# Kernel optimization log

Hardware: AMD Instinct MI355X
Metric: run time of the kernel (lower is better)

## Reference

```python
import jax, jax.numpy as jnp
import numpy as np


def setup_inputs() -> dict:
    key = jax.random.key(0)
    kx, kw = jax.random.split(key)
    B, IN, OUT = 8192, 4096, 4096
    x = jax.random.normal(kx, (B, IN), dtype=jnp.float32)
    # matches torch init: (rand*2-1)*0.001 -> uniform in [-0.001, 0.001]
    weight = jax.random.uniform(kw, (OUT, IN), dtype=jnp.float32, minval=-1.0, maxval=1.0) * 0.001
    return {"x": x, "weight": weight}


def reference(x, weight):
    # scaling factor = mean(|W|), detached
    scale = jax.lax.stop_gradient(jnp.mean(jnp.abs(weight)))
    binary_no_grad = scale * jnp.sign(weight)
    clipped = jnp.clip(weight, -1.0, 1.0)
    # straight-through estimator: fwd value = scale*sign(W), bwd grad = d(clip)/dW
    binary_weights = jax.lax.stop_gradient(binary_no_grad - clipped) + clipped
    # F.linear: y = x @ W^T  -> [B, OUT]
    return jnp.einsum('bi,oi->bo', x, binary_weights)
```

## Files before the change

### kernel.cpp

```cpp
#include <hip/hip_runtime.h>
#include <hip/hip_bf16.h>
#include <stdint.h>

typedef __attribute__((ext_vector_type(4))) int i32x4;
typedef __attribute__((ext_vector_type(4))) float f32x4;

#define GLOAD(g, l) __builtin_amdgcn_global_load_lds(                      \
    (const __attribute__((address_space(1))) void*)(g),                    \
    (__attribute__((address_space(3))) void*)(l), 16, 0, 0)

#define MFMAI8 __builtin_amdgcn_mfma_i32_16x16x64_i8
#define BARRIER __builtin_amdgcn_s_barrier

__global__ __launch_bounds__(512, 2) void gemm_i8_kernel(
    const char* __restrict__ A,
    const char* __restrict__ B,
    const float* __restrict__ partials, const float* __restrict__ qrow,
    float* __restrict__ C) {
  constexpr int M = 8192, N = 4096, K = 4096;
  constexpr int NT = K / 128;
  constexpr int NI = NT / 2;
  __shared__ __align__(16) char lds[131072];

  const int tid = threadIdx.x;
  const int wid = tid >> 6;
  const int lane = tid & 63;
  const int wr = wid >> 2;
  const int wc = wid & 3;
  const int bh = wc >> 1;
  const int bsub = (wc & 1) * 8192;
  const int fr = lane & 15;
  const int fq = lane >> 4;
  const int sk0 = ((fq) ^ (fr & 7)) * 16;
  const int sk1 = ((4 + fq) ^ (fr & 7)) * 16;

  const int bid = blockIdx.x;
  const int xcd = bid & 7;
  const int local = bid >> 3;
  const int tm = (xcd >> 1) * 8 + (local >> 3);
  const int tn = (xcd & 1) * 8 + (local & 7);

  const int srow = tid >> 3;
  const int sg = (tid & 7) ^ (srow & 7);
  const char* aSrc0 = A + (size_t)(tm * 256 + srow) * K + sg * 16;
  const char* aSrc1 = aSrc0 + (size_t)128 * K;
  const char* bSrc0 = B + (size_t)(tn * 256 + srow) * K + sg * 16;
  const char* bSrc1 = bSrc0 + (size_t)128 * K;

#define STAGE(srcBase, slotIdx, koff)                              \
  do {                                                             \
    const char* _s = (srcBase) + (koff);                           \
    char* _d = lds + (slotIdx) * 16384 + wid * 1024;               \
    GLOAD(_s, _d);                                                 \
    GLOAD(_s + (size_t)64 * K, _d + 8192);                         \
  } while (0)

  const char* aSp0 = lds + (0 + wr) * 16384 + fr * 128;
  const char* aSp1 = lds + (2 + wr) * 16384 + fr * 128;
  const char* bSp0 = lds + (4 + bh) * 16384 + bsub + fr * 128;
  const char* bSp1 = lds + (6 + bh) * 16384 + bsub + fr * 128;

  i32x4 acc[8][4];
#pragma unroll
  for (int m = 0; m < 8; ++m)
#pragma unroll
    for (int n = 0; n < 4; ++n) acc[m][n] = (i32x4){0, 0, 0, 0};

#define RD_B(bS)                                                       \
  _Pragma("unroll") for (int n = 0; n < 4; ++n) {                      \
    bq[n][0] = *(const i32x4*)((bS) + n * 2048 + sk0);                 \
    bq[n][1] = *(const i32x4*)((bS) + n * 2048 + sk1);                 \
  }
#define RD_A(dst, aS, q)                                               \
  _Pragma("unroll") for (int m2 = 0; m2 < 2; ++m2) {                   \
    dst[m2][0] = *(const i32x4*)((aS) + (2 * (q) + m2) * 2048 + sk0);  \
    dst[m2][1] = *(const i32x4*)((aS) + (2 * (q) + m2) * 2048 + sk1);  \
  }
#define QMFMA(av, q)                                                   \
  do {                                                                 \
    __builtin_amdgcn_s_setprio(1);                                     \
    _Pragma("unroll") for (int m2 = 0; m2 < 2; ++m2)                   \
        _Pragma("unroll") for (int n = 0; n < 4; ++n) {                \
      acc[2 * (q) + m2][n] =                                           \
          MFMAI8(av[m2][0], bq[n][0], acc[2 * (q) + m2][n], 0, 0, 0);  \
      acc[2 * (q) + m2][n] =                                           \
          MFMAI8(av[m2][1], bq[n][1], acc[2 * (q) + m2][n], 0, 0, 0);  \
    }                                                                  \
    __builtin_amdgcn_s_setprio(0);                                     \
  } while (0)

  STAGE(bSrc0, 4, 0);
  STAGE(bSrc1, 5, 0);
  STAGE(aSrc0, 0, 0);
  STAGE(aSrc1, 1, 0);
  STAGE(bSrc0, 6, 128);
  asm volatile("s_waitcnt vmcnt(2)" ::: "memory");
  BARRIER();

  i32x4 bq[4][2], av0[2][2], av1[2][2];
  RD_B(bSp0);
  RD_A(av0, aSp0, 0);

  for (int i = 0; i < NI; ++i) {
    const int t0 = 2 * i;
    const int k1 = (t0 + 1) * 128, k2 = (t0 + 2) * 128, k3 = (t0 + 3) * 128;

    RD_A(av1, aSp0, 1);
    STAGE(bSrc1, 7, k1);
    BARRIER();
    QMFMA(av0, 0);

    RD_A(av0, aSp0, 2);
    STAGE(aSrc0, 2, k1);
    BARRIER();
    QMFMA(av1, 1);

    RD_A(av1, aSp0, 3);
    STAGE(aSrc1, 3, k1);
    BARRIER();
    QMFMA(av0, 2);

    if (t0 + 2 < NT) {
      STAGE(bSrc0, 4, k2);
      asm volatile("s_waitcnt vmcnt(2)" ::: "memory");
    } else {
      asm volatile("s_waitcnt vmcnt(0)" ::: "memory");
    }
    BARRIER();
    QMFMA(av1, 3);
    RD_B(bSp1);
    RD_A(av0, aSp1, 0);

    RD_A(av1, aSp1, 1);
    if (t0 + 2 < NT) STAGE(bSrc1, 5, k2);
    BARRIER();
    QMFMA(av0, 0);

    RD_A(av0, aSp1, 2);
    if (t0 + 2 < NT) STAGE(aSrc0, 0, k2);
    BARRIER();
    QMFMA(av1, 1);

    RD_A(av1, aSp1, 3);
    if (t0 + 2 < NT) STAGE(aSrc1, 1, k2);
    BARRIER();
    QMFMA(av0, 2);

    if (t0 + 2 < NT) {
      STAGE(bSrc0, 6, k3);
      asm volatile("s_waitcnt vmcnt(2)" ::: "memory");
    }
    BARRIER();
    QMFMA(av1, 3);
    if (t0 + 2 < NT) {
      RD_B(bSp0);
      RD_A(av0, aSp0, 0);
    }
  }

  BARRIER();
  float s = 0.f;
  for (int i = tid; i < 4096; i += 512) s += partials[i];
#pragma unroll
  for (int off = 32; off > 0; off >>= 1) s += __shfl_down(s, off, 64);
  float* smf = reinterpret_cast<float*>(lds);
  if (lane == 0) smf[wid] = s;
  BARRIER();
  float tot = 0.f;
#pragma unroll
  for (int j = 0; j < 8; ++j) tot += smf[j];
  const float sc = tot * (1.0f / 16777216.0f);

  const int crow0 = tm * 256 + wr * 128 + fq * 4;
  const int ccol0 = tn * 256 + wc * 64 + fr;
#pragma unroll
  for (int m = 0; m < 8; ++m) {
    const int row = crow0 + m * 16;
    float q[4];
#pragma unroll
    for (int j = 0; j < 4; ++j) q[j] = sc * qrow[row + j];
#pragma unroll
    for (int n = 0; n < 4; ++n) {
      i32x4 v = acc[m][n];
      float* cp = C + (size_t)row * N + ccol0 + n * 16;
#pragma unroll
      for (int j = 0; j < 4; ++j) cp[(size_t)j * N] = (float)v[j] * q[j];
    }
  }
#undef STAGE
#undef RD_A
#undef RD_B
#undef QMFMA
}

__global__ __launch_bounds__(256) void prep_kernel(
    const float* __restrict__ X, const float* __restrict__ W,
    char* __restrict__ XQ, char* __restrict__ SQ,
    float* __restrict__ qrow, float* __restrict__ partials) {
  const int b = blockIdx.x;
  const int tid = threadIdx.x;
  if (b < 8192) {
    const int row = b;
    const f32x4* xr =
        reinterpret_cast<const f32x4*>(X + (size_t)row * 4096);
    int* xo = reinterpret_cast<int*>(XQ + (size_t)row * 4096);
    f32x4 v[4];
    float am = 0.f;
#pragma unroll
    for (int i = 0; i < 4; ++i) {
      v[i] = __builtin_nontemporal_load(xr + tid + 256 * i);
      am = fmaxf(am, fmaxf(fmaxf(fabsf(v[i][0]), fabsf(v[i][1])),
                           fmaxf(fabsf(v[i][2]), fabsf(v[i][3]))));
    }
#pragma unroll
    for (int off = 1; off < 64; off <<= 1)
      am = fmaxf(am, __shfl_xor(am, off, 64));
    __shared__ float wm[4];
    if ((tid & 63) == 0) wm[tid >> 6] = am;
    __syncthreads();
    float amax = fmaxf(fmaxf(wm[0], wm[1]), fmaxf(wm[2], wm[3]));
    amax = fmaxf(amax, 1e-20f);
    const float rq = 127.f / amax;
#pragma unroll
    for (int i = 0; i < 4; ++i) {
      int b0 = __float2int_rn(v[i][0] * rq);
      int b1 = __float2int_rn(v[i][1] * rq);
      int b2 = __float2int_rn(v[i][2] * rq);
      int b3 = __float2int_rn(v[i][3] * rq);
      xo[tid + 256 * i] = (b0 & 255) | ((b1 & 255) << 8) |
                          ((b2 & 255) << 16) | ((b3 & 255) << 24);
    }
    if (tid == 0) qrow[row] = amax * (1.f / 127.f);
  } else {
    const int base = (b - 8192) * 1024;
    const f32x4* wp = reinterpret_cast<const f32x4*>(W);
    int* sp = reinterpret_cast<int*>(SQ);
    float s = 0.f;
#pragma unroll
    for (int i = 0; i < 4; ++i) {
      const int idx = base + tid + 256 * i;
      f32x4 w = __builtin_nontemporal_load(wp + idx);
      int b0 = (w[0] > 0.f) - (w[0] < 0.f);
      int b1 = (w[1] > 0.f) - (w[1] < 0.f);
      int b2 = (w[2] > 0.f) - (w[2] < 0.f);
      int b3 = (w[3] > 0.f) - (w[3] < 0.f);
      sp[idx] = (b0 & 255) | ((b1 & 255) << 8) | ((b2 & 255) << 16) |
                ((b3 & 255) << 24);
      s += fabsf(w[0]) + fabsf(w[1]) + fabsf(w[2]) + fabsf(w[3]);
    }
#pragma unroll
    for (int off = 32; off > 0; off >>= 1) s += __shfl_down(s, off, 64);
    __shared__ float sm[4];
    if ((tid & 63) == 0) sm[tid >> 6] = s;
    __syncthreads();
    if (tid == 0) partials[b - 8192] = sm[0] + sm[1] + sm[2] + sm[3];
  }
}

extern "C" void kernel_launch(void* const* d_in, const int* in_sizes, int n_in,
                              void* d_out, int out_size, void* d_ws,
                              size_t ws_size, hipStream_t stream) {
  const float* x = (const float*)d_in[0];
  const float* w = (const float*)d_in[1];
  float* out = (float*)d_out;

  char* ws = (char*)d_ws;
  char* xq = ws;
  char* sq = ws + 33554432;
  float* qrow = (float*)(ws + 50331648);
  float* partials = (float*)(ws + 50331648 + 32768);

  prep_kernel<<<12288, 256, 0, stream>>>(x, w, xq, sq, qrow, partials);
  gemm_i8_kernel<<<512, 512, 0, stream>>>(xq, sq, partials, qrow, out);
}
```

Baseline: 161.5 us.

## Load A operand directly from global into registers, stage only B in LDS

The A tile is no longer staged through LDS. Each wave now reads its A fragments straight from global memory into registers. Only B is double-buffered in LDS, which halves the shared-memory footprint and reduces barriers to roughly two per k-step. The aim is to cut LDS traffic and synchronisation. The cost is that the four waves sharing an A row block each fetch it separately, and the per-lane 16-byte strided global reads are less coalesced, which raises L2/global load pressure and exposes more latency to the MFMA chain.

```diff
diff --git a/kernel.cpp b/kernel.cpp
--- a/kernel.cpp
+++ b/kernel.cpp
@@ -19,8 +19,7 @@
     float* __restrict__ C) {
   constexpr int M = 8192, N = 4096, K = 4096;
   constexpr int NT = K / 128;
-  constexpr int NI = NT / 2;
-  __shared__ __align__(16) char lds[131072];
+  __shared__ __align__(16) char lds[65536];
 
   const int tid = threadIdx.x;
   const int wid = tid >> 6;
@@ -42,8 +41,6 @@
 
   const int srow = tid >> 3;
   const int sg = (tid & 7) ^ (srow & 7);
-  const char* aSrc0 = A + (size_t)(tm * 256 + srow) * K + sg * 16;
-  const char* aSrc1 = aSrc0 + (size_t)128 * K;
   const char* bSrc0 = B + (size_t)(tn * 256 + srow) * K + sg * 16;
   const char* bSrc1 = bSrc0 + (size_t)128 * K;
 
@@ -55,10 +52,15 @@
     GLOAD(_s + (size_t)64 * K, _d + 8192);                         \
   } while (0)
 
-  const char* aSp0 = lds + (0 + wr) * 16384 + fr * 128;
-  const char* aSp1 = lds + (2 + wr) * 16384 + fr * 128;
-  const char* bSp0 = lds + (4 + bh) * 16384 + bsub + fr * 128;
-  const char* bSp1 = lds + (6 + bh) * 16384 + bsub + fr * 128;
+  const char* bSp0 = lds + bh * 16384 + bsub + fr * 128;
+
+  const char* aRow = A + (size_t)(tm * 256 + wr * 128 + fr) * K + fq * 16;
+
+#define LD_A(dst, q, koff)                                              \
+  _Pragma("unroll") for (int m2 = 0; m2 < 2; ++m2)                      \
+      _Pragma("unroll") for (int kk = 0; kk < 2; ++kk)                  \
+          dst[m2][kk] = *(const i32x4*)(aRow +                          \
+              (size_t)(2 * (q) + m2) * 16 * K + (koff) + kk * 64);
 
   i32x4 acc[8][4];
 #pragma unroll
@@ -70,11 +72,6 @@
   _Pragma("unroll") for (int n = 0; n < 4; ++n) {                      \
     bq[n][0] = *(const i32x4*)((bS) + n * 2048 + sk0);                 \
     bq[n][1] = *(const i32x4*)((bS) + n * 2048 + sk1);                 \
-  }
-#define RD_A(dst, aS, q)                                               \
-  _Pragma("unroll") for (int m2 = 0; m2 < 2; ++m2) {                   \
-    dst[m2][0] = *(const i32x4*)((aS) + (2 * (q) + m2) * 2048 + sk0);  \
-    dst[m2][1] = *(const i32x4*)((aS) + (2 * (q) + m2) * 2048 + sk1);  \
   }
 #define QMFMA(av, q)                                                   \
   do {                                                                 \
@@ -89,75 +86,47 @@
     __builtin_amdgcn_s_setprio(0);                                     \
   } while (0)
 
-  STAGE(bSrc0, 4, 0);
-  STAGE(bSrc1, 5, 0);
-  STAGE(aSrc0, 0, 0);
-  STAGE(aSrc1, 1, 0);
-  STAGE(bSrc0, 6, 128);
-  asm volatile("s_waitcnt vmcnt(2)" ::: "memory");
+  i32x4 bq[4][2], av0[2][2], av1[2][2];
+
+  STAGE(bSrc0, 0, 0);
+  STAGE(bSrc1, 1, 0);
+  STAGE(bSrc0, 2, 128);
+  STAGE(bSrc1, 3, 128);
+  LD_A(av0, 0, 0);
+  asm volatile("s_waitcnt vmcnt(8)" ::: "memory");
   BARRIER();
 
-  i32x4 bq[4][2], av0[2][2], av1[2][2];
-  RD_B(bSp0);
-  RD_A(av0, aSp0, 0);
-
-  for (int i = 0; i < NI; ++i) {
-    const int t0 = 2 * i;
-    const int k1 = (t0 + 1) * 128, k2 = (t0 + 2) * 128, k3 = (t0 + 3) * 128;
-
-    RD_A(av1, aSp0, 1);
-    STAGE(bSrc1, 7, k1);
+  for (int t = 0; t < NT; ++t) {
+    const int par = t & 1;
+    const char* bS = bSp0 + par * 32768;
+    const int koff = t * 128;
+
+    RD_B(bS);
+    LD_A(av1, 1, koff);
+    QMFMA(av0, 0);
+
+    LD_A(av0, 2, koff);
+    QMFMA(av1, 1);
+
     BARRIER();
-    QMFMA(av0, 0);
-
-    RD_A(av0, aSp0, 2);
-    STAGE(aSrc0, 2, k1);
-    BARRIER();
-    QMFMA(av1, 1);
-
-    RD_A(av1, aSp0, 3);
-    STAGE(aSrc1, 3, k1);
-    BARRIER();
+
+    LD_A(av1, 3, koff);
+    if (t + 2 < NT) {
+      STAGE(bSrc0, par * 2, (t + 2) * 128);
+      STAGE(bSrc1, par * 2 + 1, (t + 2) * 128);
+    }
     QMFMA(av0, 2);
 
-    if (t0 + 2 < NT) {
-      STAGE(bSrc0, 4, k2);
-      asm volatile("s_waitcnt vmcnt(2)" ::: "memory");
-    } else {
-      asm volatile("s_waitcnt vmcnt(0)" ::: "memory");
-    }
-    BARRIER();
+    if (t + 1 < NT) LD_A(av0, 0, (t + 1) * 128);
     QMFMA(av1, 3);
-    RD_B(bSp1);
-    RD_A(av0, aSp1, 0);
-
-    RD_A(av1, aSp1, 1);
-    if (t0 + 2 < NT) STAGE(bSrc1, 5, k2);
-    BARRIER();
-    QMFMA(av0, 0);
-
-    RD_A(av0, aSp1, 2);
-    if (t0 + 2 < NT) STAGE(aSrc0, 0, k2);
-    BARRIER();
-    QMFMA(av1, 1);
-
-    RD_A(av1, aSp1, 3);
-    if (t0 + 2 < NT) STAGE(aSrc1, 1, k2);
-    BARRIER();
-    QMFMA(av0, 2);
-
-    if (t0 + 2 < NT) {
-      STAGE(bSrc0, 6, k3);
-      asm volatile("s_waitcnt vmcnt(2)" ::: "memory");
-    }
-    BARRIER();
-    QMFMA(av1, 3);
-    if (t0 + 2 < NT) {
-      RD_B(bSp0);
-      RD_A(av0, aSp0, 0);
-    }
-  }
-
+
+    if (t + 1 < NT) {
+      asm volatile("s_waitcnt vmcnt(8)" ::: "memory");
+      BARRIER();
+    }
+  }
+
+  asm volatile("s_waitcnt vmcnt(0)" ::: "memory");
   BARRIER();
   float s = 0.f;
   for (int i = tid; i < 4096; i += 512) s += partials[i];
@@ -188,7 +157,7 @@
     }
   }
 #undef STAGE
-#undef RD_A
+#undef LD_A
 #undef RD_B
 #undef QMFMA
 }
```

Result: slower. 309.0 us (+91.3%).
